# Kernel tuning notes

Measured on AMD Instinct MI355X. Metric: run time of the kernel, lower is better.

Reference implementation:

```python
import jax, jax.numpy as jnp
import numpy as np

N, F_IN, H1, C1, C2, Q, E = 50000, 256, 4, 32, 128, 768, 800000
NEG_SLOPE = 0.2


def gat_layer(x, src, dst, W, a_src, a_dst, bias, heads, ch, num_nodes):
    # x: [N, F]; W: [F, heads*ch]; a_src/a_dst: [heads, ch]
    xw = (x @ W).reshape(num_nodes, heads, ch)
    alpha_s = jnp.sum(xw * a_src, axis=-1)  # [N, heads]
    alpha_d = jnp.sum(xw * a_dst, axis=-1)  # [N, heads]
    e = jax.nn.leaky_relu(alpha_s[src] + alpha_d[dst], NEG_SLOPE)  # [E, heads]
    # segment softmax over destination nodes (every node has a self-loop)
    m = jax.ops.segment_max(e, dst, num_segments=num_nodes)
    e = jnp.exp(e - m[dst])
    denom = jax.ops.segment_sum(e, dst, num_segments=num_nodes)
    alpha = e / (denom[dst] + 1e-16)  # [E, heads]
    msg = alpha[:, :, None] * xw[src]  # [E, heads, ch]
    out = jax.ops.segment_sum(msg, dst, num_segments=num_nodes)
    return out.reshape(num_nodes, heads * ch) + bias


def setup_inputs() -> dict:
    key = jax.random.key(0)
    ks = jax.random.split(key, 16)
    s = lambda fan_in: 1.0 / np.sqrt(fan_in)
    return {
        "entity_features": jax.random.normal(ks[0], (N, F_IN), jnp.float32),
        "edge_index": jax.random.randint(ks[1], (2, E), 0, N, jnp.int32),
        "question_embedding": jax.random.normal(ks[2], (Q,), jnp.float32),
        "question_entity_mask": jax.random.randint(ks[3], (N,), 0, 2, jnp.int32),
        "place_entity_mask": jax.random.randint(ks[4], (N,), 0, 2, jnp.int32),
        "W1": jax.random.normal(ks[5], (F_IN, H1 * C1), jnp.float32) * s(F_IN),
        "att_src1": jax.random.normal(ks[6], (H1, C1), jnp.float32) * s(C1),
        "att_dst1": jax.random.normal(ks[7], (H1, C1), jnp.float32) * s(C1),
        "b1": jnp.zeros((H1 * C1,), jnp.float32),
        "W2": jax.random.normal(ks[8], (H1 * C1, C2), jnp.float32) * s(H1 * C1),
        "att_src2": jax.random.normal(ks[9], (1, C2), jnp.float32) * s(C2),
        "att_dst2": jax.random.normal(ks[10], (1, C2), jnp.float32) * s(C2),
        "b2": jnp.zeros((C2,), jnp.float32),
        "Wq": jax.random.normal(ks[11], (C2 + Q, 1), jnp.float32) * s(C2 + Q),
        "bq": jnp.zeros((1,), jnp.float32),
    }


def reference(entity_features, edge_index, question_embedding, question_entity_mask,
              place_entity_mask, W1, att_src1, att_dst1, b1, W2, att_src2, att_dst2, b2, Wq, bq):
    # add self-loops (PyG GATConv default add_self_loops=True)
    loops = jnp.arange(N, dtype=edge_index.dtype)
    src = jnp.concatenate([edge_index[0], loops])
    dst = jnp.concatenate([edge_index[1], loops])

    x = gat_layer(entity_features, src, dst, W1, att_src1, att_dst1, b1, H1, C1, N)
    x = jax.nn.elu(x)  # dropout is identity in eval
    ents = gat_layer(x, src, dst, W2, att_src2, att_dst2, b2, 1, C2, N)
    ents = jax.nn.elu(ents)  # [N, C2]

    q = jnp.broadcast_to(question_embedding[None, :], (N, Q))
    combined = jnp.concatenate([ents, q], axis=-1)  # [N, C2+Q]
    logits = (combined @ Wq + bq)[:, 0]  # [N]
    logits = logits + (question_entity_mask.astype(jnp.float32) - 1.0) * 1e9
    attn = jax.nn.softmax(logits, axis=0)  # [N]
    pooled = jnp.sum(attn[:, None] * ents, axis=0)  # [C2]
    return pooled, ents, attn
```

## Files before the change

### kernel.cpp

```cpp
#include <hip/hip_runtime.h>
#include <hip/hip_fp16.h>
#include <math.h>

#define N_NODES 50000
#define F_IN    256
#define H1      4
#define C1      32
#define HC      128
#define C2      128
#define QDIM    768
#define NE      800000
#define NB_SCAN 196
#define NB_POOL 512


__device__ __forceinline__ void atomicMaxFloat(float* addr, float val) {
    if (val >= 0.f)
        atomicMax(reinterpret_cast<int*>(addr), __float_as_int(val));
    else
        atomicMin(reinterpret_cast<unsigned int*>(addr), __float_as_uint(val));
}


__global__ void init_scal_kernel(float* scal) {
    scal[1] = -INFINITY;
    scal[2] = 0.f;
}

__global__ void qdot_kernel(const float* __restrict__ q, const float* __restrict__ Wq,
                            const float* __restrict__ bq, float* scal) {
    __shared__ float sm[256];
    float acc = 0.f;
    for (int i = threadIdx.x; i < QDIM; i += 256) acc += q[i] * Wq[C2 + i];
    sm[threadIdx.x] = acc;
    __syncthreads();
    for (int o = 128; o > 0; o >>= 1) {
        if (threadIdx.x < o) sm[threadIdx.x] += sm[threadIdx.x + o];
        __syncthreads();
    }
    if (threadIdx.x == 0) scal[0] = sm[0] + bq[0];
}


__global__ void hist_kernel(const int* __restrict__ ei, int* __restrict__ deg) {
    int e = blockIdx.x * blockDim.x + threadIdx.x;
    if (e >= NE) return;
    atomicAdd(&deg[ei[NE + e]], 1);
}

__global__ void scan1_kernel(const int* __restrict__ deg, int* __restrict__ incl,
                             int* __restrict__ bsum) {
    __shared__ int sm[256];
    int i = blockIdx.x * 256 + threadIdx.x;
    int v = (i < N_NODES) ? deg[i] : 0;
    sm[threadIdx.x] = v;
    __syncthreads();
    for (int o = 1; o < 256; o <<= 1) {
        int t = (threadIdx.x >= o) ? sm[threadIdx.x - o] : 0;
        __syncthreads();
        sm[threadIdx.x] += t;
        __syncthreads();
    }
    if (i < N_NODES) incl[i] = sm[threadIdx.x];
    if (threadIdx.x == 255) bsum[blockIdx.x] = sm[255];
}

__global__ void scan2_kernel(int* __restrict__ bsum) {
    __shared__ int sm[256];
    int v = (threadIdx.x < NB_SCAN) ? bsum[threadIdx.x] : 0;
    sm[threadIdx.x] = v;
    __syncthreads();
    for (int o = 1; o < 256; o <<= 1) {
        int t = (threadIdx.x >= o) ? sm[threadIdx.x - o] : 0;
        __syncthreads();
        sm[threadIdx.x] += t;
        __syncthreads();
    }
    if (threadIdx.x < NB_SCAN) bsum[threadIdx.x] = sm[threadIdx.x] - v;
}

__global__ void scan3_kernel(const int* __restrict__ deg, const int* __restrict__ incl,
                             const int* __restrict__ bsum, int* __restrict__ rowptr,
                             int* __restrict__ cursor) {
    int i = blockIdx.x * 256 + threadIdx.x;
    if (i >= N_NODES) return;
    int excl = incl[i] - deg[i] + bsum[i >> 8];
    rowptr[i] = excl;
    cursor[i] = excl;
    if (i == N_NODES - 1) rowptr[N_NODES] = excl + deg[i];
}

__global__ void scatter_kernel(const int* __restrict__ ei, int* __restrict__ cursor,
                               int* __restrict__ colsrc) {
    int e = blockIdx.x * blockDim.x + threadIdx.x;
    if (e >= NE) return;
    int s = ei[e], d = ei[NE + e];
    int pos = atomicAdd(&cursor[d], 1);
    colsrc[pos] = s;
}


#define BM 64
#define BN 128
#define BKK 16

__global__ __launch_bounds__(256) void gemm_f32(const float* __restrict__ A,
                                                const float* __restrict__ B,
                                                __half* __restrict__ Ch,
                                                int M, int K) {
    __shared__ float As[BKK][BM + 4];
    __shared__ float Bs[BKK][BN];
    const int t  = threadIdx.x;
    const int tx = t & 15, ty = t >> 4;
    const int row0 = blockIdx.x * BM;

    const int ar  = t >> 2;
    const int akb = (t & 3) * 4;
    const int bk = t >> 5;
    const int bn = (t * 4) & 127;

    float acc[4][8] = {};

    for (int k0 = 0; k0 < K; k0 += BKK) {
        float4 av = make_float4(0.f, 0.f, 0.f, 0.f);
        if (row0 + ar < M)
            av = *reinterpret_cast<const float4*>(A + (long)(row0 + ar) * K + k0 + akb);
        As[akb + 0][ar] = av.x;
        As[akb + 1][ar] = av.y;
        As[akb + 2][ar] = av.z;
        As[akb + 3][ar] = av.w;
        *reinterpret_cast<float4*>(&Bs[bk][bn]) =
            *reinterpret_cast<const float4*>(B + (long)(k0 + bk) * BN + bn);
        *reinterpret_cast<float4*>(&Bs[bk + 8][bn]) =
            *reinterpret_cast<const float4*>(B + (long)(k0 + bk + 8) * BN + bn);
        __syncthreads();
#pragma unroll
        for (int k = 0; k < BKK; k++) {
            float4 a  = *reinterpret_cast<const float4*>(&As[k][ty * 4]);
            float4 b0 = *reinterpret_cast<const float4*>(&Bs[k][tx * 4]);
            float4 b1 = *reinterpret_cast<const float4*>(&Bs[k][64 + tx * 4]);
            float aa[4] = {a.x, a.y, a.z, a.w};
            float bb[8] = {b0.x, b0.y, b0.z, b0.w, b1.x, b1.y, b1.z, b1.w};
#pragma unroll
            for (int i = 0; i < 4; i++)
#pragma unroll
                for (int j = 0; j < 8; j++) acc[i][j] += aa[i] * bb[j];
        }
        __syncthreads();
    }
#pragma unroll
    for (int i = 0; i < 4; i++) {
        int r = row0 + ty * 4 + i;
        if (r < M) {
            union { __half2 h2[2]; uint2 u; } p0, p1;
            p0.h2[0] = __floats2half2_rn(acc[i][0], acc[i][1]);
            p0.h2[1] = __floats2half2_rn(acc[i][2], acc[i][3]);
            p1.h2[0] = __floats2half2_rn(acc[i][4], acc[i][5]);
            p1.h2[1] = __floats2half2_rn(acc[i][6], acc[i][7]);
            *reinterpret_cast<uint2*>(Ch + (long)r * BN + tx * 4)      = p0.u;
            *reinterpret_cast<uint2*>(Ch + (long)r * BN + 64 + tx * 4) = p1.u;
        }
    }
}


__global__ void alpha_kernel(const __half* __restrict__ xw,
                             const float* __restrict__ a_src,
                             const float* __restrict__ a_dst,
                             float* __restrict__ as_, float* __restrict__ ad_,
                             int NH, int H, int C) {
    int i = blockIdx.x * blockDim.x + threadIdx.x;
    if (i >= NH) return;
    int n = i / H, h = i - n * H;
    const __half2* row = reinterpret_cast<const __half2*>(xw + (long)n * HC + h * C);
    const float* vs  = a_src + h * C;
    const float* vd  = a_dst + h * C;
    float s = 0.f, d = 0.f;
    for (int k2 = 0; k2 < C / 2; k2++) {
        float2 f = __half22float2(row[k2]);
        s += f.x * vs[2 * k2] + f.y * vs[2 * k2 + 1];
        d += f.x * vd[2 * k2] + f.y * vd[2 * k2 + 1];
    }
    as_[i] = s;
    ad_[i] = d;
}


template<int H>
__global__ __launch_bounds__(256) void gat_agg_kernel(const int* __restrict__ rowptr,
                                                      const int* __restrict__ colsrc,
                                                      const float* __restrict__ as_,
                                                      const float* __restrict__ ad_,
                                                      const __half* __restrict__ xw,
                                                      const float* __restrict__ bias,
                                                      float* __restrict__ outbuf,
                                                      int fuse_elu) {
    constexpr int CHUNK = 64 / H;
    int n    = (blockIdx.x * blockDim.x + threadIdx.x) >> 6;
    int lane = threadIdx.x & 63;
    if (n >= N_NODES) return;
    const int h_my  = lane / CHUNK;
    const int eslot = lane & (CHUNK - 1);
    const int l16   = lane & 15;
    const int grp   = lane >> 4;
    const int cbase = l16 * 8;
    const int hg    = (H == 1) ? 0 : (cbase >> 5);

    const float adn = ad_[n * H + h_my];
    float m;
    {
        float v = as_[n * H + h_my] + adn;
        m = (v > 0.f) ? v : 0.2f * v;
    }
    float den = 1.f;

    float acc[8] = {};
    if (grp == 0) {
        union { uint4 u; __half2 h[4]; } cv;
        cv.u = *reinterpret_cast<const uint4*>(xw + (long)n * HC + cbase);
#pragma unroll
        for (int k = 0; k < 4; k++) {
            float2 f = __half22float2(cv.h[k]);
            acc[2 * k]     = f.x;
            acc[2 * k + 1] = f.y;
        }
    }

    const int rbeg = rowptr[n], rend = rowptr[n + 1];
    for (int base = rbeg; base < rend; base += CHUNK) {
        int idx = base + eslot;
        int s   = (idx < rend) ? colsrc[idx] : -1;
        float ev;
        if (s >= 0) {
            float v = as_[(long)s * H + h_my] + adn;
            ev = (v > 0.f) ? v : 0.2f * v;
        } else {
            ev = -INFINITY;
        }
        float cm = ev;
#pragma unroll
        for (int o = CHUNK / 2; o > 0; o >>= 1) cm = fmaxf(cm, __shfl_xor(cm, o));
        float nm = fmaxf(m, cm);
        float sc = __expf(m - nm);
        den *= sc;
        m = nm;
        float e_ = (s >= 0) ? __expf(ev - nm) : 0.f;
        float ssum = e_;
#pragma unroll
        for (int o = CHUNK / 2; o > 0; o >>= 1) ssum += __shfl_xor(ssum, o);
        den += ssum;
        float sc_g = (H == 1) ? sc : __shfl(sc, hg * CHUNK);
#pragma unroll
        for (int k = 0; k < 8; k++) acc[k] *= sc_g;
        int cnt = min(CHUNK, rend - base);
#pragma unroll 4
        for (int j4 = 0; j4 < cnt; j4 += 4) {
            int eidx = j4 + grp;
            int   sj = __shfl(s,  eidx);
            float aj = __shfl(e_, hg * CHUNK + eidx);
            int  sjc = (sj < 0) ? 0 : sj;
            union { uint4 u; __half2 h[4]; } cv;
            cv.u = *reinterpret_cast<const uint4*>(xw + (long)sjc * HC + cbase);
#pragma unroll
            for (int k = 0; k < 4; k++) {
                float2 f = __half22float2(cv.h[k]);
                acc[2 * k]     += aj * f.x;
                acc[2 * k + 1] += aj * f.y;
            }
        }
    }

#pragma unroll
    for (int k = 0; k < 8; k++) {
        acc[k] += __shfl_xor(acc[k], 16);
        acc[k] += __shfl_xor(acc[k], 32);
    }
    float den_g = (H == 1) ? den : __shfl(den, hg * CHUNK);
    if (grp == 0) {
        float inv = 1.f / (den_g + 1e-16f);
        float o[8];
#pragma unroll
        for (int k = 0; k < 8; k++) {
            float v = acc[k] * inv;
            if (fuse_elu) {
                v += bias[cbase + k];
                v = (v > 0.f) ? v : (__expf(v) - 1.f);
            }
            o[k] = v;
        }
        float4 o0 = make_float4(o[0], o[1], o[2], o[3]);
        float4 o1 = make_float4(o[4], o[5], o[6], o[7]);
        *reinterpret_cast<float4*>(outbuf + (long)n * HC + cbase)     = o0;
        *reinterpret_cast<float4*>(outbuf + (long)n * HC + cbase + 4) = o1;
    }
}


__global__ __launch_bounds__(256) void ents_logits_kernel(float* __restrict__ ents,
                                                          const float* __restrict__ b2,
                                                          const float* __restrict__ Wq,
                                                          const int* __restrict__ qmask,
                                                          const float* __restrict__ scal,
                                                          float* __restrict__ logits) {
    int wid  = (blockIdx.x * blockDim.x + threadIdx.x) >> 6;
    int lane = threadIdx.x & 63;
    if (wid >= N_NODES) return;
    int c = lane * 2;
    float2 v = *reinterpret_cast<float2*>(ents + (long)wid * HC + c);
    float x0 = v.x + b2[c], x1 = v.y + b2[c + 1];
    x0 = (x0 > 0.f) ? x0 : (__expf(x0) - 1.f);
    x1 = (x1 > 0.f) ? x1 : (__expf(x1) - 1.f);
    float2 w; w.x = x0; w.y = x1;
    *reinterpret_cast<float2*>(ents + (long)wid * HC + c) = w;
    float acc = x0 * Wq[c] + x1 * Wq[c + 1];
#pragma unroll
    for (int o = 32; o > 0; o >>= 1) acc += __shfl_down(acc, o);
    if (lane == 0)
        logits[wid] = acc + scal[0] + ((float)qmask[wid] - 1.f) * 1e9f;
}

__global__ __launch_bounds__(256) void red_max_kernel(const float* __restrict__ logits,
                                                      float* scal) {
    __shared__ float sm[256];
    float mx = -INFINITY;
    for (int i = blockIdx.x * 256 + threadIdx.x; i < N_NODES; i += gridDim.x * 256)
        mx = fmaxf(mx, logits[i]);
    sm[threadIdx.x] = mx;
    __syncthreads();
    for (int o = 128; o > 0; o >>= 1) {
        if (threadIdx.x < o) sm[threadIdx.x] = fmaxf(sm[threadIdx.x], sm[threadIdx.x + o]);
        __syncthreads();
    }
    if (threadIdx.x == 0) atomicMaxFloat(&scal[1], sm[0]);
}

__global__ __launch_bounds__(256) void red_sum_kernel(float* __restrict__ logits,
                                                      float* scal) {
    __shared__ float sm[256];
    const float gmax = scal[1];
    float acc = 0.f;
    for (int i = blockIdx.x * 256 + threadIdx.x; i < N_NODES; i += gridDim.x * 256) {
        float ex = __expf(logits[i] - gmax);
        logits[i] = ex;
        acc += ex;
    }
    sm[threadIdx.x] = acc;
    __syncthreads();
    for (int o = 128; o > 0; o >>= 1) {
        if (threadIdx.x < o) sm[threadIdx.x] += sm[threadIdx.x + o];
        __syncthreads();
    }
    if (threadIdx.x == 0) unsafeAtomicAdd(&scal[2], sm[0]);
}

__global__ void attn_kernel(const float* __restrict__ logits, const float* __restrict__ scal,
                            float* __restrict__ attn_out) {
    int n = blockIdx.x * blockDim.x + threadIdx.x;
    if (n >= N_NODES) return;
    attn_out[n] = logits[n] / scal[2];
}

__global__ __launch_bounds__(128) void pooled_partial_kernel(const float* __restrict__ ents,
                                                             const float* __restrict__ attn,
                                                             float* __restrict__ partial) {
    int c = threadIdx.x;
    float acc = 0.f;
    for (int n = blockIdx.x; n < N_NODES; n += gridDim.x)
        acc += attn[n] * ents[(long)n * HC + c];
    partial[(long)blockIdx.x * HC + c] = acc;
}

__global__ __launch_bounds__(128) void pooled_reduce_kernel(const float* __restrict__ partial,
                                                            float* __restrict__ pooled) {
    int c = threadIdx.x;
    float acc = 0.f;
    for (int b = 0; b < NB_POOL; b++) acc += partial[(long)b * HC + c];
    pooled[c] = acc;
}


extern "C" void kernel_launch(void* const* d_in, const int* in_sizes, int n_in,
                              void* d_out, int out_size, void* d_ws, size_t ws_size,
                              hipStream_t stream) {
    const float* x     = (const float*)d_in[0];
    const int*   ei    = (const int*)d_in[1];
    const float* q     = (const float*)d_in[2];
    const int*   qmask = (const int*)d_in[3];
    const float* W1    = (const float*)d_in[5];
    const float* asrc1 = (const float*)d_in[6];
    const float* adst1 = (const float*)d_in[7];
    const float* b1    = (const float*)d_in[8];
    const float* W2    = (const float*)d_in[9];
    const float* asrc2 = (const float*)d_in[10];
    const float* adst2 = (const float*)d_in[11];
    const float* b2    = (const float*)d_in[12];
    const float* Wq    = (const float*)d_in[13];
    const float* bq    = (const float*)d_in[14];

    float* out    = (float*)d_out;
    float* pooled = out;
    float* ents   = out + HC;
    float* attn   = out + HC + (long)N_NODES * HC;

    float*  ws     = (float*)d_ws;
    __half* xw     = (__half*)ws;
    float* as1     = ws + (long)N_NODES * HC / 2;
    float* ad1     = as1 + N_NODES * H1;
    float* as2     = ad1 + N_NODES * H1;
    float* ad2     = as2 + N_NODES;
    float* logits  = ad2 + N_NODES;
    float* scal    = logits + N_NODES;
    float* partial = scal + 4;
    int*   deg     = (int*)(partial + NB_POOL * HC);
    int*   incl    = deg + N_NODES;
    int*   bsum    = incl + N_NODES;
    int*   rowptr  = bsum + 256;
    int*   cursor  = rowptr + N_NODES + 1;
    int*   colsrc  = cursor + N_NODES;

    const int TB = 256;
    const int g_nh1 = (N_NODES * H1 + TB - 1) / TB;
    const int g_n   = (N_NODES + TB - 1) / TB;
    const int g_e   = (NE + TB - 1) / TB;
    const int g_nw  = (N_NODES + 3) / 4;
    const int g_gemm = (N_NODES + BM - 1) / BM;

    hipMemsetAsync(deg, 0, N_NODES * sizeof(int), stream);
    init_scal_kernel<<<1, 1, 0, stream>>>(scal);
    qdot_kernel<<<1, TB, 0, stream>>>(q, Wq, bq, scal);

    hist_kernel<<<g_e, TB, 0, stream>>>(ei, deg);
    scan1_kernel<<<NB_SCAN, TB, 0, stream>>>(deg, incl, bsum);
    scan2_kernel<<<1, TB, 0, stream>>>(bsum);
    scan3_kernel<<<NB_SCAN, TB, 0, stream>>>(deg, incl, bsum, rowptr, cursor);
    scatter_kernel<<<g_e, TB, 0, stream>>>(ei, cursor, colsrc);

    gemm_f32<<<g_gemm, TB, 0, stream>>>(x, W1, xw, N_NODES, F_IN);
    alpha_kernel<<<g_nh1, TB, 0, stream>>>(xw, asrc1, adst1, as1, ad1, N_NODES * H1, H1, C1);
    gat_agg_kernel<H1><<<g_nw, TB, 0, stream>>>(rowptr, colsrc, as1, ad1, xw, b1, ents, 1);

    gemm_f32<<<g_gemm, TB, 0, stream>>>(ents, W2, xw, N_NODES, HC);
    alpha_kernel<<<g_n, TB, 0, stream>>>(xw, asrc2, adst2, as2, ad2, N_NODES, 1, C2);
    gat_agg_kernel<1><<<g_nw, TB, 0, stream>>>(rowptr, colsrc, as2, ad2, xw, b2, ents, 0);

    ents_logits_kernel<<<g_nw, TB, 0, stream>>>(ents, b2, Wq, qmask, scal, logits);
    red_max_kernel<<<NB_SCAN, TB, 0, stream>>>(logits, scal);
    red_sum_kernel<<<NB_SCAN, TB, 0, stream>>>(logits, scal);
    attn_kernel<<<g_n, TB, 0, stream>>>(logits, scal, attn);
    pooled_partial_kernel<<<NB_POOL, 128, 0, stream>>>(ents, attn, partial);
    pooled_reduce_kernel<<<1, 128, 0, stream>>>(partial, pooled);
}
```

Baseline: 482.4 us.

## Partition scatter by destination range per XCD and prefetch GEMM tiles into registers

The CSR scatter kernel now assigns each block to one of eight destination-node ranges, chosen by blockIdx modulo 8, and walks the edge list with a grid-stride loop. The aim is that atomics on cursor and writes to colsrc for a given range land in one XCD's L2, assuming round-robin block placement. In exchange every block reads the whole destination array, so edge reads go up eightfold. Separately, the fp32 GEMM loads the next K-tile of A and B into registers before the current tile's compute, so global load latency overlaps the FMA loop at some register cost.

Result: faster. 467.8 us (-3.0%).

```diff
diff --git a/kernel.cpp b/kernel.cpp
--- a/kernel.cpp
+++ b/kernel.cpp
@@ -12,6 +12,8 @@
 #define NE      800000
 #define NB_SCAN 196
 #define NB_POOL 512
+#define NXCD    8
+#define DST_RANGE ((N_NODES + NXCD - 1) / NXCD)
 
 
 __device__ __forceinline__ void atomicMaxFloat(float* addr, float val) {
@@ -92,11 +94,17 @@
 
 __global__ void scatter_kernel(const int* __restrict__ ei, int* __restrict__ cursor,
                                int* __restrict__ colsrc) {
-    int e = blockIdx.x * blockDim.x + threadIdx.x;
-    if (e >= NE) return;
-    int s = ei[e], d = ei[NE + e];
-    int pos = atomicAdd(&cursor[d], 1);
-    colsrc[pos] = s;
+    const int range = blockIdx.x & (NXCD - 1);
+    const int lo = range * DST_RANGE, hi = lo + DST_RANGE;
+    const int nb = gridDim.x >> 3;
+    const int slice = blockIdx.x >> 3;
+    for (int e = slice * blockDim.x + threadIdx.x; e < NE; e += nb * blockDim.x) {
+        int d = ei[NE + e];
+        if (d >= lo && d < hi) {
+            int pos = atomicAdd(&cursor[d], 1);
+            colsrc[pos] = ei[e];
+        }
+    }
 }
 
 
@@ -118,22 +126,30 @@
     const int akb = (t & 3) * 4;
     const int bk = t >> 5;
     const int bn = (t * 4) & 127;
+    const bool arow_ok = (row0 + ar < M);
 
     float acc[4][8] = {};
 
+    float4 av = make_float4(0.f, 0.f, 0.f, 0.f);
+    if (arow_ok)
+        av = *reinterpret_cast<const float4*>(A + (long)(row0 + ar) * K + akb);
+    float4 bv0 = *reinterpret_cast<const float4*>(B + (long)bk * BN + bn);
+    float4 bv1 = *reinterpret_cast<const float4*>(B + (long)(bk + 8) * BN + bn);
+
     for (int k0 = 0; k0 < K; k0 += BKK) {
-        float4 av = make_float4(0.f, 0.f, 0.f, 0.f);
-        if (row0 + ar < M)
-            av = *reinterpret_cast<const float4*>(A + (long)(row0 + ar) * K + k0 + akb);
         As[akb + 0][ar] = av.x;
         As[akb + 1][ar] = av.y;
         As[akb + 2][ar] = av.z;
         As[akb + 3][ar] = av.w;
-        *reinterpret_cast<float4*>(&Bs[bk][bn]) =
-            *reinterpret_cast<const float4*>(B + (long)(k0 + bk) * BN + bn);
-        *reinterpret_cast<float4*>(&Bs[bk + 8][bn]) =
-            *reinterpret_cast<const float4*>(B + (long)(k0 + bk + 8) * BN + bn);
-        __syncthreads();
+        *reinterpret_cast<float4*>(&Bs[bk][bn]) = bv0;
+        *reinterpret_cast<float4*>(&Bs[bk + 8][bn]) = bv1;
+        __syncthreads();
+        if (k0 + BKK < K) {
+            if (arow_ok)
+                av = *reinterpret_cast<const float4*>(A + (long)(row0 + ar) * K + k0 + BKK + akb);
+            bv0 = *reinterpret_cast<const float4*>(B + (long)(k0 + BKK + bk) * BN + bn);
+            bv1 = *reinterpret_cast<const float4*>(B + (long)(k0 + BKK + bk + 8) * BN + bn);
+        }
 #pragma unroll
         for (int k = 0; k < BKK; k++) {
             float4 a  = *reinterpret_cast<const float4*>(&As[k][ty * 4]);
@@ -424,6 +440,7 @@
     const int g_e   = (NE + TB - 1) / TB;
     const int g_nw  = (N_NODES + 3) / 4;
     const int g_gemm = (N_NODES + BM - 1) / BM;
+    const int g_scat = 2048;
 
     hipMemsetAsync(deg, 0, N_NODES * sizeof(int), stream);
     init_scal_kernel<<<1, 1, 0, stream>>>(scal);
@@ -433,7 +450,7 @@
     scan1_kernel<<<NB_SCAN, TB, 0, stream>>>(deg, incl, bsum);
     scan2_kernel<<<1, TB, 0, stream>>>(bsum);
     scan3_kernel<<<NB_SCAN, TB, 0, stream>>>(deg, incl, bsum, rowptr, cursor);
-    scatter_kernel<<<g_e, TB, 0, stream>>>(ei, cursor, colsrc);
+    scatter_kernel<<<g_scat, TB, 0, stream>>>(ei, cursor, colsrc);
 
     gemm_f32<<<g_gemm, TB, 0, stream>>>(x, W1, xw, N_NODES, F_IN);
     alpha_kernel<<<g_nh1, TB, 0, stream>>>(xw, asrc1, adst1, as1, ad1, N_NODES * H1, H1, C1);
```
